# Kernel optimization log

Hardware: AMD Instinct MI355X
Metric: run time of the kernel (lower is better)

Reference implementation:

```python
import jax, jax.numpy as jnp
import numpy as np

# SE3 transform stored as [..., 7] = [quat(wxyz), translation(xyz)]

def qmul(a, b):
    w1, x1, y1, z1 = a[..., 0], a[..., 1], a[..., 2], a[..., 3]
    w2, x2, y2, z2 = b[..., 0], b[..., 1], b[..., 2], b[..., 3]
    return jnp.stack([
        w1 * w2 - x1 * x2 - y1 * y2 - z1 * z2,
        w1 * x2 + x1 * w2 + y1 * z2 - z1 * y2,
        w1 * y2 - x1 * z2 + y1 * w2 + z1 * x2,
        w1 * z2 + x1 * y2 - y1 * x2 + z1 * w2,
    ], axis=-1)


def qrot(q, v):
    # rotate vectors v [...,3] by unit quaternions q [...,4] (wxyz)
    qv, w = q[..., 1:], q[..., 0:1]
    t = 2.0 * jnp.cross(qv, v)
    return v + w * t + jnp.cross(qv, t)


def se3_mul(Ta, Tb):
    qa, ta = Ta[..., :4], Ta[..., 4:]
    qb, tb = Tb[..., :4], Tb[..., 4:]
    return jnp.concatenate([qmul(qa, qb), qrot(qa, tb) + ta], axis=-1)


def se3_inv(T):
    q, t = T[..., :4], T[..., 4:]
    qi = q * jnp.array([1.0, -1.0, -1.0, -1.0], dtype=q.dtype)
    return jnp.concatenate([qi, -qrot(qi, t)], axis=-1)


def _rand_se3(key, n):
    kq, kt = jax.random.split(key)
    q = jax.random.normal(kq, (n, 4), dtype=jnp.float32)
    q = q / jnp.linalg.norm(q, axis=-1, keepdims=True)
    t = jax.random.normal(kt, (n, 3), dtype=jnp.float32)
    return jnp.concatenate([q, t], axis=-1)


def setup_inputs() -> dict:
    E, B = 500000, 64
    node_dim = edge_dim = global_dim = hidden_dim = 128
    DIM = 7
    in_dim = 2 * node_dim + DIM + edge_dim + global_dim  # 519
    key = jax.random.key(0)
    ks = jax.random.split(key, 12)
    return {
        "xfeati": jax.random.normal(ks[0], (E, node_dim), dtype=jnp.float32),
        "xfeatj": jax.random.normal(ks[1], (E, node_dim), dtype=jnp.float32),
        "edge_feat": jax.random.normal(ks[2], (E, edge_dim), dtype=jnp.float32),
        "Ti": _rand_se3(ks[3], E),
        "Tj": _rand_se3(ks[4], E),
        "Tij_hat": _rand_se3(ks[5], E),
        "u": jax.random.normal(ks[6], (B, global_dim), dtype=jnp.float32),
        "batch": jax.random.randint(ks[7], (E,), 0, B, dtype=jnp.int32),
        "W1": jax.random.normal(ks[8], (in_dim, hidden_dim), dtype=jnp.float32) / np.sqrt(in_dim),
        "b1": jnp.zeros((hidden_dim,), dtype=jnp.float32),
        "W2": jax.random.normal(ks[9], (hidden_dim, edge_dim), dtype=jnp.float32) / np.sqrt(hidden_dim),
        "b2": jnp.zeros((edge_dim,), dtype=jnp.float32),
    }


def reference(xfeati, xfeatj, edge_feat, Ti, Tj, Tij_hat, u, batch, W1, b1, W2, b2):
    Tij = se3_mul(Tj, se3_inv(Ti))         # [E, 7]
    T_err = se3_mul(Tij_hat, se3_inv(Tij))  # [E, 7] -> .vec()
    feat_cat = jnp.concatenate([xfeati, xfeatj, edge_feat, T_err, u[batch]], axis=1)
    h = jax.nn.relu(feat_cat @ W1 + b1)
    edge_feat_out = edge_feat + (h @ W2 + b2)
    return (edge_feat_out, Tij_hat)
```

## Files before the change

### kernel.cpp

```cpp
#include <hip/hip_runtime.h>

typedef __attribute__((ext_vector_type(4))) float f32x4;
typedef __attribute__((ext_vector_type(8))) short bf16x8;

__device__ __forceinline__ unsigned short f2bf(float f){
  unsigned int x = __float_as_uint(f);
  return (unsigned short)((x + 0x7fffu + ((x >> 16) & 1u)) >> 16);
}

__device__ __forceinline__ unsigned int cvt2(float lo, float hi){
  unsigned int r;
  asm("v_cvt_pk_bf16_f32 %0, %1, %2" : "=v"(r) : "v"(lo), "v"(hi));
  return r;
}

struct Q  { float w,x,y,z; };
struct V3 { float x,y,z; };
struct M3 { float m[9]; };

__device__ __forceinline__ Q qmul(Q a, Q b){
  return { a.w*b.w - a.x*b.x - a.y*b.y - a.z*b.z,
           a.w*b.x + a.x*b.w + a.y*b.z - a.z*b.y,
           a.w*b.y - a.x*b.z + a.y*b.w + a.z*b.x,
           a.w*b.z + a.x*b.y - a.y*b.x + a.z*b.w };
}
__device__ __forceinline__ Q qconj(Q q){ return { q.w, -q.x, -q.y, -q.z }; }
__device__ __forceinline__ M3 q2R(Q q){
  const float w=q.w, x=q.x, y=q.y, z=q.z;
  M3 R;
  R.m[0]=1.f-2.f*(y*y+z*z); R.m[1]=2.f*(x*y-w*z);     R.m[2]=2.f*(x*z+w*y);
  R.m[3]=2.f*(x*y+w*z);     R.m[4]=1.f-2.f*(x*x+z*z); R.m[5]=2.f*(y*z-w*x);
  R.m[6]=2.f*(x*z-w*y);     R.m[7]=2.f*(y*z+w*x);     R.m[8]=1.f-2.f*(x*x+y*y);
  return R;
}
__device__ __forceinline__ V3 mv (M3 R, V3 v){
  return { R.m[0]*v.x + R.m[1]*v.y + R.m[2]*v.z,
           R.m[3]*v.x + R.m[4]*v.y + R.m[5]*v.z,
           R.m[6]*v.x + R.m[7]*v.y + R.m[8]*v.z };
}
__device__ __forceinline__ V3 mtv(M3 R, V3 v){
  return { R.m[0]*v.x + R.m[3]*v.y + R.m[6]*v.z,
           R.m[1]*v.x + R.m[4]*v.y + R.m[7]*v.z,
           R.m[2]*v.x + R.m[5]*v.y + R.m[8]*v.z };
}

__global__ void prep_kernel(const float* __restrict__ W1, const float* __restrict__ W2,
                            unsigned short* __restrict__ W1p, unsigned short* __restrict__ W2p){
  const int N1 = 128*544;
  int gid = blockIdx.x*256 + threadIdx.x;
  if (gid < N1){
    int c = gid / 544, k = gid % 544;
    W1p[gid] = (k < 519) ? f2bf(W1[(size_t)k*128 + c]) : (unsigned short)0;
  } else if (gid < N1 + 128*128){
    int g = gid - N1;
    int c = g >> 7, k = g & 127;
    W2p[g] = f2bf(W2[(size_t)k*128 + c]);
  }
}

template<bool WSP>
__global__ __launch_bounds__(512) void edge_k(
    const float* __restrict__ xfi, const float* __restrict__ xfj, const float* __restrict__ ef,
    const float* __restrict__ Ti,  const float* __restrict__ Tj,  const float* __restrict__ Th,
    const int*   __restrict__ batch, const float* __restrict__ u,
    const float* __restrict__ W1,  const float* __restrict__ b1,
    const float* __restrict__ W2,  const float* __restrict__ b2,
    const unsigned short* __restrict__ W1p, const unsigned short* __restrict__ W2p,
    float* __restrict__ outE, float* __restrict__ outT, int E)
{
  __shared__ __align__(16) unsigned short tailb[64][168];
  __shared__ __align__(16) unsigned short fbuf[64][136];
  __shared__ __align__(16) unsigned short hbf[64][136];
  __shared__ int ibat_s[64];

  const int tid = threadIdx.x;
  const long base = (long)blockIdx.x * 64;

  if (tid < 64){
    const long row = base + tid;
    const long rc  = row < E ? row : (long)(E-1);
    const float* pi = Ti + rc*7;
    const float* pj = Tj + rc*7;
    const float* ph = Th + rc*7;
    Q  qi{pi[0],pi[1],pi[2],pi[3]};  V3 tti{pi[4],pi[5],pi[6]};
    Q  qj{pj[0],pj[1],pj[2],pj[3]};  V3 ttj{pj[4],pj[5],pj[6]};
    Q  qh{ph[0],ph[1],ph[2],ph[3]};  V3 tth{ph[4],ph[5],ph[6]};
    M3 Ri = q2R(qi), Rj = q2R(qj), Rh = q2R(qh);
    V3 a  = mtv(Rj, ttj);
    V3 bv = mv(Ri, a);
    V3 c  { tti.x - bv.x, tti.y - bv.y, tti.z - bv.z };
    V3 d  = mv(Rh, c);
    Q  qe = qmul(qmul(qh, qi), qconj(qj));
    tailb[tid][0] = f2bf(qe.w);
    tailb[tid][1] = f2bf(qe.x);
    tailb[tid][2] = f2bf(qe.y);
    tailb[tid][3] = f2bf(qe.z);
    tailb[tid][4] = f2bf(tth.x + d.x);
    tailb[tid][5] = f2bf(tth.y + d.y);
    tailb[tid][6] = f2bf(tth.z + d.z);
    ibat_s[tid] = batch[rc];
    if (row < E){
      float* o = outT + row*7;
      o[0]=ph[0]; o[1]=ph[1]; o[2]=ph[2]; o[3]=ph[3];
      o[4]=ph[4]; o[5]=ph[5]; o[6]=ph[6];
    }
  }
  __syncthreads();

  for (int idx = tid; idx < 64*128; idx += 512){
    const int e = idx >> 7, c = idx & 127;
    tailb[e][7 + c] = f2bf(u[(size_t)ibat_s[e]*128 + c]);
  }
  for (int idx = tid; idx < 64*33; idx += 512){
    const int e = idx / 33, c = idx % 33;
    tailb[e][135 + c] = 0;
  }

  const int lane = tid & 63, wv = tid >> 6;
  const int l15 = lane & 15, l4 = lane >> 4;
  const int col = wv*16 + l15;

  f32x4 acc1[4];
  {
    const float bv = b1[col];
    #pragma unroll
    for (int a = 0; a < 4; ++a){
      #pragma unroll
      for (int r = 0; r < 4; ++r) acc1[a][r] = bv;
    }
  }

  const float* fps[3] = { xfi, xfj, ef };
  for (int fb = 0; fb < 3; ++fb){
    const float* F = fps[fb];
    __syncthreads();
    #pragma unroll
    for (int i = 0; i < 4; ++i){
      const int idx = i*512 + tid;
      const int e = idx >> 5, c4 = (idx & 31) << 2;
      long rr = base + e; if (rr >= E) rr = E-1;
      const float4 v = *reinterpret_cast<const float4*>(F + (size_t)rr*128 + c4);
      unsigned int* dst = reinterpret_cast<unsigned int*>(&fbuf[e][c4]);
      dst[0] = cvt2(v.x, v.y);
      dst[1] = cvt2(v.z, v.w);
    }
    __syncthreads();
    #pragma unroll
    for (int kc = 0; kc < 4; ++kc){
      const int kl = kc*32 + l4*8;
      bf16x8 afr[4];
      #pragma unroll
      for (int a = 0; a < 4; ++a)
        afr[a] = *reinterpret_cast<const bf16x8*>(&fbuf[a*16 + l15][kl]);
      bf16x8 Bv;
      if (WSP){
        Bv = *reinterpret_cast<const bf16x8*>(W1p + (size_t)col*544 + fb*128 + kl);
      } else {
        float w[8];
        #pragma unroll
        for (int j = 0; j < 8; ++j){
          const int kk = fb*128 + kl + j;
          w[j] = W1[(size_t)kk*128 + col];
        }
        union { bf16x8 v; unsigned int ui[4]; } B;
        B.ui[0] = cvt2(w[0], w[1]);
        B.ui[1] = cvt2(w[2], w[3]);
        B.ui[2] = cvt2(w[4], w[5]);
        B.ui[3] = cvt2(w[6], w[7]);
        Bv = B.v;
      }
      #pragma unroll
      for (int a = 0; a < 4; ++a)
        acc1[a] = __builtin_amdgcn_mfma_f32_16x16x32_bf16(afr[a], Bv, acc1[a], 0, 0, 0);
    }
  }
  #pragma unroll
  for (int tc = 0; tc < 5; ++tc){
    const int kt = tc*32 + l4*8;
    bf16x8 afr[4];
    #pragma unroll
    for (int a = 0; a < 4; ++a)
      afr[a] = *reinterpret_cast<const bf16x8*>(&tailb[a*16 + l15][kt]);
    bf16x8 Bv;
    if (WSP){
      Bv = *reinterpret_cast<const bf16x8*>(W1p + (size_t)col*544 + 384 + kt);
    } else {
      float w[8];
      #pragma unroll
      for (int j = 0; j < 8; ++j){
        const int kk = 384 + kt + j;
        w[j] = (kk < 519) ? W1[(size_t)kk*128 + col] : 0.f;
      }
      union { bf16x8 v; unsigned int ui[4]; } B;
      B.ui[0] = cvt2(w[0], w[1]);
      B.ui[1] = cvt2(w[2], w[3]);
      B.ui[2] = cvt2(w[4], w[5]);
      B.ui[3] = cvt2(w[6], w[7]);
      Bv = B.v;
    }
    #pragma unroll
    for (int a = 0; a < 4; ++a)
      acc1[a] = __builtin_amdgcn_mfma_f32_16x16x32_bf16(afr[a], Bv, acc1[a], 0, 0, 0);
  }

  #pragma unroll
  for (int a = 0; a < 4; ++a){
    #pragma unroll
    for (int r = 0; r < 4; ++r)
      hbf[a*16 + l4*4 + r][col] = f2bf(fmaxf(acc1[a][r], 0.f));
  }
  __syncthreads();

  f32x4 acc2[4];
  {
    const float bv2 = b2[col];
    #pragma unroll
    for (int a = 0; a < 4; ++a){
      #pragma unroll
      for (int r = 0; r < 4; ++r){
        long orow = base + a*16 + l4*4 + r;
        if (orow >= E) orow = E-1;
        acc2[a][r] = ef[(size_t)orow*128 + col] + bv2;
      }
    }
  }
  #pragma unroll
  for (int ks = 0; ks < 4; ++ks){
    const int k0 = ks*32 + l4*8;
    bf16x8 afr[4];
    #pragma unroll
    for (int a = 0; a < 4; ++a)
      afr[a] = *reinterpret_cast<const bf16x8*>(&hbf[a*16 + l15][k0]);
    bf16x8 Bv;
    if (WSP){
      Bv = *reinterpret_cast<const bf16x8*>(W2p + (size_t)col*128 + k0);
    } else {
      float w[8];
      #pragma unroll
      for (int j = 0; j < 8; ++j)
        w[j] = W2[(size_t)(k0 + j)*128 + col];
      union { bf16x8 v; unsigned int ui[4]; } B;
      B.ui[0] = cvt2(w[0], w[1]);
      B.ui[1] = cvt2(w[2], w[3]);
      B.ui[2] = cvt2(w[4], w[5]);
      B.ui[3] = cvt2(w[6], w[7]);
      Bv = B.v;
    }
    #pragma unroll
    for (int a = 0; a < 4; ++a)
      acc2[a] = __builtin_amdgcn_mfma_f32_16x16x32_bf16(afr[a], Bv, acc2[a], 0, 0, 0);
  }

  #pragma unroll
  for (int a = 0; a < 4; ++a){
    #pragma unroll
    for (int r = 0; r < 4; ++r){
      const long orow = base + a*16 + l4*4 + r;
      if (orow < E) outE[(size_t)orow*128 + col] = acc2[a][r];
    }
  }
}

extern "C" void kernel_launch(void* const* d_in, const int* in_sizes, int n_in,
                              void* d_out, int out_size, void* d_ws, size_t ws_size,
                              hipStream_t stream){
  const float* xfi  = (const float*)d_in[0];
  const float* xfj  = (const float*)d_in[1];
  const float* ef   = (const float*)d_in[2];
  const float* Ti   = (const float*)d_in[3];
  const float* Tj   = (const float*)d_in[4];
  const float* Th   = (const float*)d_in[5];
  const float* u    = (const float*)d_in[6];
  const int*   bat  = (const int*)d_in[7];
  const float* W1   = (const float*)d_in[8];
  const float* b1   = (const float*)d_in[9];
  const float* W2   = (const float*)d_in[10];
  const float* b2   = (const float*)d_in[11];
  const int E = in_sizes[0] / 128;

  float* outE = (float*)d_out;
  float* outT = outE + (size_t)E * 128;

  const int grid = (E + 63) / 64;
  const size_t need = (size_t)(128*544 + 128*128) * sizeof(unsigned short);
  if (d_ws != nullptr && ws_size >= need){
    unsigned short* W1p = (unsigned short*)d_ws;
    unsigned short* W2p = W1p + (size_t)128*544;
    prep_kernel<<<(128*544 + 128*128 + 255)/256, 256, 0, stream>>>(W1, W2, W1p, W2p);
    edge_k<true><<<grid, 512, 0, stream>>>(xfi, xfj, ef, Ti, Tj, Th, bat, u,
                                           W1, b1, W2, b2, W1p, W2p, outE, outT, E);
  } else {
    edge_k<false><<<grid, 512, 0, stream>>>(xfi, xfj, ef, Ti, Tj, Th, bat, u,
                                            W1, b1, W2, b2, nullptr, nullptr, outE, outT, E);
  }
}
```

Baseline: 284.0 us.

## Double-buffer feature tiles and prefetch next block during MFMA

```diff
diff --git a/kernel.cpp b/kernel.cpp
--- a/kernel.cpp
+++ b/kernel.cpp
@@ -69,7 +69,7 @@
     float* __restrict__ outE, float* __restrict__ outT, int E)
 {
   __shared__ __align__(16) unsigned short tailb[64][168];
-  __shared__ __align__(16) unsigned short fbuf[64][136];
+  __shared__ __align__(16) unsigned short fbuf[2][64][136];
   __shared__ __align__(16) unsigned short hbf[64][136];
   __shared__ int ibat_s[64];
 
@@ -107,9 +107,13 @@
   }
   __syncthreads();
 
-  for (int idx = tid; idx < 64*128; idx += 512){
-    const int e = idx >> 7, c = idx & 127;
-    tailb[e][7 + c] = f2bf(u[(size_t)ibat_s[e]*128 + c]);
+  for (int idx = tid; idx < 64*32; idx += 512){
+    const int e = idx >> 5, q = idx & 31;
+    const float4 v = *reinterpret_cast<const float4*>(u + (size_t)ibat_s[e]*128 + q*4);
+    const unsigned int p01 = cvt2(v.x, v.y), p23 = cvt2(v.z, v.w);
+    unsigned short* d = &tailb[e][7 + q*4];
+    d[0] = (unsigned short)p01; d[1] = (unsigned short)(p01 >> 16);
+    d[2] = (unsigned short)p23; d[3] = (unsigned short)(p23 >> 16);
   }
   for (int idx = tid; idx < 64*33; idx += 512){
     const int e = idx / 33, c = idx % 33;
@@ -120,6 +124,9 @@
   const int l15 = lane & 15, l4 = lane >> 4;
   const int col = wv*16 + l15;
 
+  const int se  = tid >> 3;
+  const int sc4 = (tid & 7) * 16;
+
   f32x4 acc1[4];
   {
     const float bv = b1[col];
@@ -131,37 +138,44 @@
   }
 
   const float* fps[3] = { xfi, xfj, ef };
+  long rr0 = base + se; if (rr0 >= E) rr0 = E-1;
+  const size_t rowb = (size_t)rr0 * 128;
+
+  {
+    const float4* src = reinterpret_cast<const float4*>(xfi + rowb + sc4);
+    unsigned int* dst = reinterpret_cast<unsigned int*>(&fbuf[0][se][sc4]);
+    #pragma unroll
+    for (int i = 0; i < 4; ++i){
+      const float4 v = src[i];
+      dst[2*i+0] = cvt2(v.x, v.y);
+      dst[2*i+1] = cvt2(v.z, v.w);
+    }
+  }
+  __syncthreads();
+
+  #pragma unroll
   for (int fb = 0; fb < 3; ++fb){
-    const float* F = fps[fb];
-    __syncthreads();
-    #pragma unroll
-    for (int i = 0; i < 4; ++i){
-      const int idx = i*512 + tid;
-      const int e = idx >> 5, c4 = (idx & 31) << 2;
-      long rr = base + e; if (rr >= E) rr = E-1;
-      const float4 v = *reinterpret_cast<const float4*>(F + (size_t)rr*128 + c4);
-      unsigned int* dst = reinterpret_cast<unsigned int*>(&fbuf[e][c4]);
-      dst[0] = cvt2(v.x, v.y);
-      dst[1] = cvt2(v.z, v.w);
-    }
-    __syncthreads();
+    float4 pre[4];
+    if (fb < 2){
+      const float4* src = reinterpret_cast<const float4*>(fps[fb+1] + rowb + sc4);
+      #pragma unroll
+      for (int i = 0; i < 4; ++i) pre[i] = src[i];
+    }
     #pragma unroll
     for (int kc = 0; kc < 4; ++kc){
       const int kl = kc*32 + l4*8;
       bf16x8 afr[4];
       #pragma unroll
       for (int a = 0; a < 4; ++a)
-        afr[a] = *reinterpret_cast<const bf16x8*>(&fbuf[a*16 + l15][kl]);
+        afr[a] = *reinterpret_cast<const bf16x8*>(&fbuf[fb&1][a*16 + l15][kl]);
       bf16x8 Bv;
       if (WSP){
         Bv = *reinterpret_cast<const bf16x8*>(W1p + (size_t)col*544 + fb*128 + kl);
       } else {
         float w[8];
         #pragma unroll
-        for (int j = 0; j < 8; ++j){
-          const int kk = fb*128 + kl + j;
-          w[j] = W1[(size_t)kk*128 + col];
-        }
+        for (int j = 0; j < 8; ++j)
+          w[j] = W1[(size_t)(fb*128 + kl + j)*128 + col];
         union { bf16x8 v; unsigned int ui[4]; } B;
         B.ui[0] = cvt2(w[0], w[1]);
         B.ui[1] = cvt2(w[2], w[3]);
@@ -173,7 +187,17 @@
       for (int a = 0; a < 4; ++a)
         acc1[a] = __builtin_amdgcn_mfma_f32_16x16x32_bf16(afr[a], Bv, acc1[a], 0, 0, 0);
     }
-  }
+    if (fb < 2){
+      unsigned int* dst = reinterpret_cast<unsigned int*>(&fbuf[(fb&1)^1][se][sc4]);
+      #pragma unroll
+      for (int i = 0; i < 4; ++i){
+        dst[2*i+0] = cvt2(pre[i].x, pre[i].y);
+        dst[2*i+1] = cvt2(pre[i].z, pre[i].w);
+      }
+    }
+    __syncthreads();
+  }
+
   #pragma unroll
   for (int tc = 0; tc < 5; ++tc){
     const int kt = tc*32 + l4*8;
```

New measurement: 341.6 us. 20.3% more time.
